# Kernel tuning notes

Measured on AMD Instinct MI355X. Metric: run time of the kernel, lower is better.

The kernel has to match this reference:

```python
import jax, jax.numpy as jnp
import numpy as np

N_NODES = 10000
N_EDGES = 640000
D_IN = 128
D_OUT = 128


def setup_inputs() -> dict:
    key = jax.random.key(0)
    k_x, k_val, k_w, k_row, k_col = jax.random.split(key, 5)
    # Glorot init for weight, zeros for bias (matches _weight_init)
    limit = float(np.sqrt(6.0 / (D_IN + D_OUT)))
    weight = jax.random.uniform(k_w, (D_IN, D_OUT), jnp.float32, -limit, limit)
    return {
        "x": jax.random.normal(k_x, (N_NODES, D_IN), jnp.float32),
        "adj_val": jax.random.uniform(k_val, (N_EDGES,), jnp.float32),  # normalized edge weights of sparse adj
        "weight": weight,
        "bias": jnp.zeros((D_OUT,), jnp.float32),
        "adj_row": jax.random.randint(k_row, (N_EDGES,), 0, N_NODES, jnp.int32),
        "adj_col": jax.random.randint(k_col, (N_EDGES,), 0, N_NODES, jnp.int32),
    }


def reference(x, adj_val, weight, bias, adj_row, adj_col):
    # dense GEMM: h = x @ W  -> [N, D_OUT]
    h = jnp.matmul(x, weight)
    # SpMM with COO adjacency: out[r] = sum_{e: row[e]=r} val[e] * h[col[e]]
    msg = adj_val[:, None] * h[adj_col]  # [E, D_OUT] gather + scale
    out = jax.ops.segment_sum(msg, adj_row, num_segments=x.shape[0])
    return out + bias
```

## Files before the change

### kernel.cpp

```cpp
#include <hip/hip_runtime.h>

#define N_NODES 10000
#define N_EDGES 640000
#define D 128
#define NQ (N_EDGES / 4)

#define NCHUNK 128
#define QPC (NQ / NCHUNK)
#define GEMM_BLOCKS 157
#define GRID1 (NCHUNK + GEMM_BLOCKS)
#define NBUCK 1250
#define CCAP 16
#define BSLOTS (NCHUNK * CCAP)
#define SPILLCAP 5000
#define CAP2 128
#define QPAD2 144
#define LSTR 136

typedef unsigned int uint32;
typedef unsigned long long u64;
typedef unsigned short u16;
using short8 = __attribute__((ext_vector_type(8))) short;
using f32x4  = __attribute__((ext_vector_type(4))) float;

__device__ __forceinline__ uint32 f2bf_bits(float f) {
    uint32 u = __float_as_uint(f);
    return (u + 0x7FFFu + ((u >> 16) & 1u)) >> 16;
}
__device__ __forceinline__ uint32 pack2(float lo, float hi) {
    return f2bf_bits(lo) | (f2bf_bits(hi) << 16);
}

__global__ __launch_bounds__(256, 4) void gemm_scatter_kernel(
    const float* __restrict__ x, const float* __restrict__ w,
    const int* __restrict__ row, const int* __restrict__ col,
    const float* __restrict__ val,
    uint32* __restrict__ h2, int* __restrict__ cnts,
    int* __restrict__ spillcnt, uint2* __restrict__ bstore,
    uint2* __restrict__ spill)
{
    __shared__ __align__(16) u16 Ws[128 * LSTR];
    const int t = threadIdx.x;

    if (blockIdx.x < NCHUNK) {
        int* lcnt = (int*)Ws;
        for (int i = t; i <= NBUCK; i += 256) lcnt[i] = 0;
        __syncthreads();

        const int sb = blockIdx.x;
        const int4*   row4 = (const int4*)row;
        const int4*   col4 = (const int4*)col;
        const float4* val4 = (const float4*)val;
        const int i0 = sb * QPC;
        for (int i = i0 + t; i < i0 + QPC; i += 256) {
            int4 r = row4[i]; int4 c = col4[i]; float4 v = val4[i];
            #pragma unroll
            for (int e = 0; e < 4; ++e) {
                int rr = (e == 0) ? r.x : (e == 1) ? r.y : (e == 2) ? r.z : r.w;
                int cc = (e == 0) ? c.x : (e == 1) ? c.y : (e == 2) ? c.z : c.w;
                float vv = (e == 0) ? v.x : (e == 1) ? v.y : (e == 2) ? v.z : v.w;
                uint32 rc = (uint32)cc | (f2bf_bits(vv) << 16);
                int b = rr >> 3;
                int k = atomicAdd(&lcnt[b], 1);
                if (k < CCAP)
                    bstore[((size_t)(b * NCHUNK + sb) << 4) + k] =
                        make_uint2(rc, (uint32)rr);
                else {
                    int ks = atomicAdd(&lcnt[NBUCK], 1);
                    spill[(size_t)sb * SPILLCAP + ks] = make_uint2(rc, (uint32)rr);
                }
            }
        }
        __syncthreads();
        for (int b = t; b < NBUCK; b += 256) {
            int c = lcnt[b];
            cnts[b * NCHUNK + sb] = (c < CCAP) ? c : CCAP;
        }
        if (t == 0) spillcnt[sb] = lcnt[NBUCK];
    } else {
        const int g = blockIdx.x - NCHUNK;
        const int lane = t & 63;
        const int wid  = t >> 6;
        const int q = lane >> 4, cl = lane & 15;

        const float4* w4 = (const float4*)w;
        #pragma unroll
        for (int i = 0; i < 8; ++i) {
            int lin = t + i * 256;
            int m  = lin >> 5;
            int qc = lin & 31;
            float4 r0 = w4[(2 * m) * 32 + qc];
            float4 r1 = w4[(2 * m + 1) * 32 + qc];
            int c = qc * 4;
            *(uint32*)&Ws[(c + 0) * LSTR + 2 * m] = pack2(r0.x, r1.x);
            *(uint32*)&Ws[(c + 1) * LSTR + 2 * m] = pack2(r0.y, r1.y);
            *(uint32*)&Ws[(c + 2) * LSTR + 2 * m] = pack2(r0.z, r1.z);
            *(uint32*)&Ws[(c + 3) * LSTR + 2 * m] = pack2(r0.w, r1.w);
        }

        int gr = g * 64 + wid * 16 + cl;
        if (gr >= N_NODES) gr = N_NODES - 1;
        const float* xrow = &x[(size_t)gr * D];
        float4 xv[8];
        #pragma unroll
        for (int kk = 0; kk < 4; ++kk) {
            xv[2 * kk]     = *(const float4*)&xrow[kk * 32 + q * 8];
            xv[2 * kk + 1] = *(const float4*)&xrow[kk * 32 + q * 8 + 4];
        }
        __syncthreads();

        f32x4 acc[8] = {};
        #pragma unroll
        for (int kk = 0; kk < 4; ++kk) {
            union { short8 s; uint32 u[4]; } af;
            float4 a = xv[2 * kk], b = xv[2 * kk + 1];
            af.u[0] = pack2(a.x, a.y); af.u[1] = pack2(a.z, a.w);
            af.u[2] = pack2(b.x, b.y); af.u[3] = pack2(b.z, b.w);
            #pragma unroll
            for (int ct = 0; ct < 8; ++ct) {
                short8 bf = *(const short8*)&Ws[(ct * 16 + cl) * LSTR + kk * 32 + q * 8];
                acc[ct] = __builtin_amdgcn_mfma_f32_16x16x32_bf16(af.s, bf, acc[ct], 0, 0, 0);
            }
        }
        #pragma unroll
        for (int reg = 0; reg < 4; ++reg) {
            int node = g * 64 + wid * 16 + q * 4 + reg;
            if (node < N_NODES) {
                uint32* base = h2 + (size_t)node * 64 + cl;
                #pragma unroll
                for (int ct = 0; ct < 4; ++ct)
                    base[ct * 16] = pack2(acc[ct][reg], acc[ct + 4][reg]);
            }
        }
    }
}

__global__ __launch_bounds__(256) void spmm_kernel(
    const uint2* __restrict__ bstore, const int* __restrict__ cnts,
    const int* __restrict__ spillcnt, const uint2* __restrict__ spill,
    const uint32* __restrict__ h2, const float* __restrict__ bias,
    float* __restrict__ out)
{
    __shared__ uint32 qbuf[8 * QPAD2];
    __shared__ int lcnts[NCHUNK];
    __shared__ int sany;
    const int t = threadIdx.x;
    const int lane = t & 63;
    const int wid  = t >> 6;
    const int b  = blockIdx.x;
    const int r0 = b * 8;

    if (t == 0) sany = 0;
    __syncthreads();
    if (t < NCHUNK) {
        lcnts[t] = cnts[b * NCHUNK + t];
        if (spillcnt[t] != 0) atomicAdd(&sany, 1);
    }
    __syncthreads();

    const size_t sbase = (size_t)b * BSLOTS;
    const uint32 da = (uint32)(wid * 2), db = da + 1;
    uint32* qa = &qbuf[(wid * 2) * QPAD2];
    uint32* qz = &qbuf[(wid * 2 + 1) * QPAD2];
    int ca = 0, cb = 0;
    const u64 pre = (lane == 63) ? ~0ull >> 1 : (1ull << lane) - 1;
    #pragma unroll 4
    for (int i = lane; i < BSLOTS; i += 64) {
        int ch = i >> 4, sl = i & 15;
        uint32 rec = 0, d = 0xFFFFFFFFu;
        if (sl < lcnts[ch]) {
            uint2 e = bstore[sbase + i];
            rec = e.x; d = e.y - (uint32)r0;
        }
        u64 ma = __ballot(d == da);
        u64 mb = __ballot(d == db);
        if (d == da) { int p = ca + __popcll(ma & pre); if (p < CAP2) qa[p] = rec; }
        if (d == db) { int p = cb + __popcll(mb & pre); if (p < CAP2) qz[p] = rec; }
        ca += __popcll(ma); cb += __popcll(mb);
    }
    if (sany) {
        for (int ch = 0; ch < NCHUNK; ++ch) {
            int sc = spillcnt[ch];
            for (int k = 0; k < sc; ++k) {
                uint2 e = spill[(size_t)ch * SPILLCAP + k];
                if (e.y == (uint32)r0 + da) { if (lane == 0 && ca < CAP2) qa[ca] = e.x; ca++; }
                if (e.y == (uint32)r0 + db) { if (lane == 0 && cb < CAP2) qz[cb] = e.x; cb++; }
            }
        }
    }

    for (int half = 0; half < 2; ++half) {
        const int r = r0 + wid * 2 + half;
        uint32* qp = (half == 0) ? qa : qz;
        const int ntot = (half == 0) ? ca : cb;
        float a0 = 0.f, a1 = 0.f;

        if (ntot <= CAP2) {
            if (lane < 16) qp[ntot + lane] = 0;
            __builtin_amdgcn_s_waitcnt(0);

            const int npad = (ntot + 7) & ~7;
            uint32 rq0,rq1,rq2,rq3,rq4,rq5,rq6,rq7;
            uint32 hh0,hh1,hh2,hh3,hh4,hh5,hh6,hh7;
            rq0 = qp[0]; hh0 = h2[((rq0 & 0xFFFFu) << 6) + lane];
            rq1 = qp[1]; hh1 = h2[((rq1 & 0xFFFFu) << 6) + lane];
            rq2 = qp[2]; hh2 = h2[((rq2 & 0xFFFFu) << 6) + lane];
            rq3 = qp[3]; hh3 = h2[((rq3 & 0xFFFFu) << 6) + lane];
            rq4 = qp[4]; hh4 = h2[((rq4 & 0xFFFFu) << 6) + lane];
            rq5 = qp[5]; hh5 = h2[((rq5 & 0xFFFFu) << 6) + lane];
            rq6 = qp[6]; hh6 = h2[((rq6 & 0xFFFFu) << 6) + lane];
            rq7 = qp[7]; hh7 = h2[((rq7 & 0xFFFFu) << 6) + lane];

#define CONSUME_PREFETCH(RQ, HH, P)                                          \
    {                                                                        \
        a0 = fmaf(__uint_as_float(RQ & 0xFFFF0000u),                         \
                  __uint_as_float(HH << 16), a0);                            \
        a1 = fmaf(__uint_as_float(RQ & 0xFFFF0000u),                         \
                  __uint_as_float(HH & 0xFFFF0000u), a1);                    \
        uint32 rn = qp[j + 8 + P];                                           \
        RQ = rn; HH = h2[((rn & 0xFFFFu) << 6) + lane];                      \
    }

            for (int j = 0; j < npad; j += 8) {
                CONSUME_PREFETCH(rq0, hh0, 0)
                CONSUME_PREFETCH(rq1, hh1, 1)
                CONSUME_PREFETCH(rq2, hh2, 2)
                CONSUME_PREFETCH(rq3, hh3, 3)
                CONSUME_PREFETCH(rq4, hh4, 4)
                CONSUME_PREFETCH(rq5, hh5, 5)
                CONSUME_PREFETCH(rq6, hh6, 6)
                CONSUME_PREFETCH(rq7, hh7, 7)
            }
#undef CONSUME_PREFETCH
        } else {
            for (int i = 0; i < BSLOTS; ++i) {
                int ch = i >> 4, sl = i & 15;
                if (sl < lcnts[ch]) {
                    uint2 e = bstore[sbase + i];
                    if (e.y == (uint32)r) {
                        uint32 hv = h2[((e.x & 0xFFFFu) << 6) + lane];
                        a0 = fmaf(__uint_as_float(e.x & 0xFFFF0000u),
                                  __uint_as_float(hv << 16), a0);
                        a1 = fmaf(__uint_as_float(e.x & 0xFFFF0000u),
                                  __uint_as_float(hv & 0xFFFF0000u), a1);
                    }
                }
            }
            for (int ch = 0; ch < NCHUNK; ++ch) {
                int sc = spillcnt[ch];
                for (int k = 0; k < sc; ++k) {
                    uint2 e = spill[(size_t)ch * SPILLCAP + k];
                    if (e.y == (uint32)r) {
                        uint32 hv = h2[((e.x & 0xFFFFu) << 6) + lane];
                        a0 = fmaf(__uint_as_float(e.x & 0xFFFF0000u),
                                  __uint_as_float(hv << 16), a0);
                        a1 = fmaf(__uint_as_float(e.x & 0xFFFF0000u),
                                  __uint_as_float(hv & 0xFFFF0000u), a1);
                    }
                }
            }
        }

        out[(size_t)r * D + lane]      = a0 + bias[lane];
        out[(size_t)r * D + 64 + lane] = a1 + bias[lane + 64];
    }
}

extern "C" void kernel_launch(void* const* d_in, const int* in_sizes, int n_in,
                              void* d_out, int out_size, void* d_ws, size_t ws_size,
                              hipStream_t stream)
{
    const float* x    = (const float*)d_in[0];
    const float* aval = (const float*)d_in[1];
    const float* w    = (const float*)d_in[2];
    const float* bias = (const float*)d_in[3];
    const int* arow   = (const int*)d_in[4];
    const int* acol   = (const int*)d_in[5];

    char* ws = (char*)d_ws;
    uint32* h2       = (uint32*)(ws);
    int*    cnts     = (int*)(ws + 2560000);
    int*    spillcnt = (int*)(ws + 3200000);
    uint2*  bstore   = (uint2*)(ws + 3200512);
    uint2*  spill    = (uint2*)(ws + 23680512);

    gemm_scatter_kernel<<<GRID1, 256, 0, stream>>>(
        x, w, arow, acol, aval, h2, cnts, spillcnt, bstore, spill);
    spmm_kernel<<<NBUCK, 256, 0, stream>>>(
        bstore, cnts, spillcnt, spill, h2, bias, (float*)d_out);
}
```

Baseline: 111.2 us.

## Bin edges per destination row with byte counts and scan-based queue build

The scatter phase now keeps a full per-row histogram in shared memory and writes 4-byte records into per-row, per-chunk cells of capacity 8, with byte-sized counts. The chunk count drops to 64 and the spill capacity is raised. The SpMM kernel then builds each row's queue with a wave prefix scan over the 64 chunk counts and two vector loads per lane. This replaces the old scan of 2048 bucket slots with ballot filtering, which cuts the record bytes read and the filtering work in the second kernel. The cost is a 40 KB shared histogram in the first kernel, which may lower occupancy for the GEMM blocks that share the kernel, plus a larger count array to write and zero.

```diff
diff --git a/kernel.cpp b/kernel.cpp
--- a/kernel.cpp
+++ b/kernel.cpp
@@ -5,14 +5,12 @@
 #define D 128
 #define NQ (N_EDGES / 4)
 
-#define NCHUNK 128
+#define NCHUNK 64
 #define QPC (NQ / NCHUNK)
 #define GEMM_BLOCKS 157
 #define GRID1 (NCHUNK + GEMM_BLOCKS)
-#define NBUCK 1250
-#define CCAP 16
-#define BSLOTS (NCHUNK * CCAP)
-#define SPILLCAP 5000
+#define RCAP 8
+#define SPILLCAP 10000
 #define CAP2 128
 #define QPAD2 144
 #define LSTR 136
@@ -20,6 +18,7 @@
 typedef unsigned int uint32;
 typedef unsigned long long u64;
 typedef unsigned short u16;
+typedef unsigned char u8;
 using short8 = __attribute__((ext_vector_type(8))) short;
 using f32x4  = __attribute__((ext_vector_type(4))) float;
 
@@ -35,16 +34,18 @@
     const float* __restrict__ x, const float* __restrict__ w,
     const int* __restrict__ row, const int* __restrict__ col,
     const float* __restrict__ val,
-    uint32* __restrict__ h2, int* __restrict__ cnts,
-    int* __restrict__ spillcnt, uint2* __restrict__ bstore,
+    uint32* __restrict__ h2, u8* __restrict__ cnts2,
+    int* __restrict__ spillcnt, uint32* __restrict__ bstore,
     uint2* __restrict__ spill)
 {
-    __shared__ __align__(16) u16 Ws[128 * LSTR];
+    __shared__ __align__(16) int SH[N_NODES];
+    __shared__ int spillc;
     const int t = threadIdx.x;
 
     if (blockIdx.x < NCHUNK) {
-        int* lcnt = (int*)Ws;
-        for (int i = t; i <= NBUCK; i += 256) lcnt[i] = 0;
+        int* hist = SH;
+        for (int i = t; i < N_NODES; i += 256) hist[i] = 0;
+        if (t == 0) spillc = 0;
         __syncthreads();
 
         const int sb = blockIdx.x;
@@ -60,24 +61,23 @@
                 int cc = (e == 0) ? c.x : (e == 1) ? c.y : (e == 2) ? c.z : c.w;
                 float vv = (e == 0) ? v.x : (e == 1) ? v.y : (e == 2) ? v.z : v.w;
                 uint32 rc = (uint32)cc | (f2bf_bits(vv) << 16);
-                int b = rr >> 3;
-                int k = atomicAdd(&lcnt[b], 1);
-                if (k < CCAP)
-                    bstore[((size_t)(b * NCHUNK + sb) << 4) + k] =
-                        make_uint2(rc, (uint32)rr);
+                int k = atomicAdd(&hist[rr], 1);
+                if (k < RCAP)
+                    bstore[(size_t)rr * (NCHUNK * RCAP) + sb * RCAP + k] = rc;
                 else {
-                    int ks = atomicAdd(&lcnt[NBUCK], 1);
+                    int ks = atomicAdd(&spillc, 1);
                     spill[(size_t)sb * SPILLCAP + ks] = make_uint2(rc, (uint32)rr);
                 }
             }
         }
         __syncthreads();
-        for (int b = t; b < NBUCK; b += 256) {
-            int c = lcnt[b];
-            cnts[b * NCHUNK + sb] = (c < CCAP) ? c : CCAP;
-        }
-        if (t == 0) spillcnt[sb] = lcnt[NBUCK];
+        for (int r = t; r < N_NODES; r += 256) {
+            int c = hist[r];
+            cnts2[(size_t)sb * N_NODES + r] = (u8)((c < RCAP) ? c : RCAP);
+        }
+        if (t == 0) spillcnt[sb] = spillc;
     } else {
+        u16* Ws = (u16*)SH;
         const int g = blockIdx.x - NCHUNK;
         const int lane = t & 63;
         const int wid  = t >> 6;
@@ -136,65 +136,58 @@
 }
 
 __global__ __launch_bounds__(256) void spmm_kernel(
-    const uint2* __restrict__ bstore, const int* __restrict__ cnts,
+    const uint32* __restrict__ bstore, const u8* __restrict__ cnts2,
     const int* __restrict__ spillcnt, const uint2* __restrict__ spill,
     const uint32* __restrict__ h2, const float* __restrict__ bias,
     float* __restrict__ out)
 {
     __shared__ uint32 qbuf[8 * QPAD2];
-    __shared__ int lcnts[NCHUNK];
-    __shared__ int sany;
     const int t = threadIdx.x;
     const int lane = t & 63;
     const int wid  = t >> 6;
-    const int b  = blockIdx.x;
-    const int r0 = b * 8;
-
-    if (t == 0) sany = 0;
-    __syncthreads();
-    if (t < NCHUNK) {
-        lcnts[t] = cnts[b * NCHUNK + t];
-        if (spillcnt[t] != 0) atomicAdd(&sany, 1);
-    }
-    __syncthreads();
-
-    const size_t sbase = (size_t)b * BSLOTS;
-    const uint32 da = (uint32)(wid * 2), db = da + 1;
-    uint32* qa = &qbuf[(wid * 2) * QPAD2];
-    uint32* qz = &qbuf[(wid * 2 + 1) * QPAD2];
-    int ca = 0, cb = 0;
-    const u64 pre = (lane == 63) ? ~0ull >> 1 : (1ull << lane) - 1;
-    #pragma unroll 4
-    for (int i = lane; i < BSLOTS; i += 64) {
-        int ch = i >> 4, sl = i & 15;
-        uint32 rec = 0, d = 0xFFFFFFFFu;
-        if (sl < lcnts[ch]) {
-            uint2 e = bstore[sbase + i];
-            rec = e.x; d = e.y - (uint32)r0;
-        }
-        u64 ma = __ballot(d == da);
-        u64 mb = __ballot(d == db);
-        if (d == da) { int p = ca + __popcll(ma & pre); if (p < CAP2) qa[p] = rec; }
-        if (d == db) { int p = cb + __popcll(mb & pre); if (p < CAP2) qz[p] = rec; }
-        ca += __popcll(ma); cb += __popcll(mb);
-    }
-    if (sany) {
-        for (int ch = 0; ch < NCHUNK; ++ch) {
-            int sc = spillcnt[ch];
-            for (int k = 0; k < sc; ++k) {
-                uint2 e = spill[(size_t)ch * SPILLCAP + k];
-                if (e.y == (uint32)r0 + da) { if (lane == 0 && ca < CAP2) qa[ca] = e.x; ca++; }
-                if (e.y == (uint32)r0 + db) { if (lane == 0 && cb < CAP2) qz[cb] = e.x; cb++; }
-            }
-        }
-    }
+    const int r0 = blockIdx.x * 8;
+
+    const bool anyspill = __ballot(spillcnt[lane & 63] != 0) != 0ull;
 
     for (int half = 0; half < 2; ++half) {
         const int r = r0 + wid * 2 + half;
-        uint32* qp = (half == 0) ? qa : qz;
-        const int ntot = (half == 0) ? ca : cb;
+        uint32* qp = &qbuf[(wid * 2 + half) * QPAD2];
+
+        int c = cnts2[(size_t)lane * N_NODES + r];
+        int p = c;
+        #pragma unroll
+        for (int d = 1; d < 64; d <<= 1) {
+            int v = __shfl_up(p, d);
+            if (lane >= d) p += v;
+        }
+        int ntot = __shfl(p, 63);
+        int base = p - c;
+        const uint32* cell = &bstore[(size_t)r * (NCHUNK * RCAP) + lane * RCAP];
+        uint4 c0 = *(const uint4*)cell;
+        uint4 c1 = *(const uint4*)(cell + 4);
+        if (c > 0 && base + 0 < CAP2) qp[base + 0] = c0.x;
+        if (c > 1 && base + 1 < CAP2) qp[base + 1] = c0.y;
+        if (c > 2 && base + 2 < CAP2) qp[base + 2] = c0.z;
+        if (c > 3 && base + 3 < CAP2) qp[base + 3] = c0.w;
+        if (c > 4 && base + 4 < CAP2) qp[base + 4] = c1.x;
+        if (c > 5 && base + 5 < CAP2) qp[base + 5] = c1.y;
+        if (c > 6 && base + 6 < CAP2) qp[base + 6] = c1.z;
+        if (c > 7 && base + 7 < CAP2) qp[base + 7] = c1.w;
+
+        if (anyspill) {
+            for (int ch = 0; ch < NCHUNK; ++ch) {
+                int sc = spillcnt[ch];
+                for (int k = 0; k < sc; ++k) {
+                    uint2 e = spill[(size_t)ch * SPILLCAP + k];
+                    if (e.y == (uint32)r) {
+                        if (lane == 0 && ntot < CAP2) qp[ntot] = e.x;
+                        ntot++;
+                    }
+                }
+            }
+        }
+
         float a0 = 0.f, a1 = 0.f;
-
         if (ntot <= CAP2) {
             if (lane < 16) qp[ntot + lane] = 0;
             __builtin_amdgcn_s_waitcnt(0);
@@ -233,17 +226,15 @@
             }
 #undef CONSUME_PREFETCH
         } else {
-            for (int i = 0; i < BSLOTS; ++i) {
-                int ch = i >> 4, sl = i & 15;
-                if (sl < lcnts[ch]) {
-                    uint2 e = bstore[sbase + i];
-                    if (e.y == (uint32)r) {
-                        uint32 hv = h2[((e.x & 0xFFFFu) << 6) + lane];
-                        a0 = fmaf(__uint_as_float(e.x & 0xFFFF0000u),
-                                  __uint_as_float(hv << 16), a0);
-                        a1 = fmaf(__uint_as_float(e.x & 0xFFFF0000u),
-                                  __uint_as_float(hv & 0xFFFF0000u), a1);
-                    }
+            for (int ch = 0; ch < NCHUNK; ++ch) {
+                int c2 = cnts2[(size_t)ch * N_NODES + r];
+                for (int k = 0; k < c2; ++k) {
+                    uint32 rec = bstore[(size_t)r * (NCHUNK * RCAP) + ch * RCAP + k];
+                    uint32 hv = h2[((rec & 0xFFFFu) << 6) + lane];
+                    a0 = fmaf(__uint_as_float(rec & 0xFFFF0000u),
+                              __uint_as_float(hv << 16), a0);
+                    a1 = fmaf(__uint_as_float(rec & 0xFFFF0000u),
+                              __uint_as_float(hv & 0xFFFF0000u), a1);
                 }
             }
             for (int ch = 0; ch < NCHUNK; ++ch) {
@@ -279,13 +270,13 @@
 
     char* ws = (char*)d_ws;
     uint32* h2       = (uint32*)(ws);
-    int*    cnts     = (int*)(ws + 2560000);
+    u8*     cnts2    = (u8*)(ws + 2560000);
     int*    spillcnt = (int*)(ws + 3200000);
-    uint2*  bstore   = (uint2*)(ws + 3200512);
+    uint32* bstore   = (uint32*)(ws + 3200512);
     uint2*  spill    = (uint2*)(ws + 23680512);
 
     gemm_scatter_kernel<<<GRID1, 256, 0, stream>>>(
-        x, w, arow, acol, aval, h2, cnts, spillcnt, bstore, spill);
-    spmm_kernel<<<NBUCK, 256, 0, stream>>>(
-        bstore, cnts, spillcnt, spill, h2, bias, (float*)d_out);
-}
+        x, w, arow, acol, aval, h2, cnts2, spillcnt, bstore, spill);
+    spmm_kernel<<<N_NODES / 8, 256, 0, stream>>>(
+        bstore, cnts2, spillcnt, spill, h2, bias, (float*)d_out);
+}
```

New measurement: 105.5 us. 5.1% less time.
